# Performance work log

Hardware: AMD Instinct MI355X
Metric: run time of the kernel (lower is better)

## Reference

```python
import jax, jax.numpy as jnp
import numpy as np

BLOCKSIZE = 64  # bitsandbytes default quantization block size

# NF4 codebook (bitsandbytes normal-float 4-bit quantiles)
NF4_CODE = jnp.array([
    -1.0, -0.6961928009986877, -0.5250730514526367, -0.39491748809814453,
    -0.28444138169288635, -0.18477343022823334, -0.09105003625154495, 0.0,
    0.07958029955625534, 0.16093020141124725, 0.24611230194568634,
    0.33791524171829224, 0.44070982933044434, 0.5626170039176941,
    0.7229568362236023, 1.0], dtype=jnp.float32)

IN_FEATURES = 4096
OUT_FEATURES = 16384
TOKENS = 8192  # batch 4 * seq 2048, flattened


def setup_inputs() -> dict:
    key = jax.random.key(0)
    k1, k2, k3, k4 = jax.random.split(key, 4)
    x = jax.random.normal(k1, (TOKENS, IN_FEATURES), dtype=jnp.float32)
    codes = jax.random.randint(k2, (OUT_FEATURES, IN_FEATURES), 0, 16, dtype=jnp.int32)
    n_blocks = OUT_FEATURES * IN_FEATURES // BLOCKSIZE
    absmax = jax.random.uniform(k3, (n_blocks,), dtype=jnp.float32)
    bias = jax.random.normal(k4, (OUT_FEATURES,), dtype=jnp.float32)
    return {"x": x, "codes": codes, "absmax": absmax, "bias": bias}


def _dequant_nf4(codes, absmax):
    # codes: [O, I] int in [0,16); absmax: [O*I/BLOCKSIZE] per-block scale
    O, I = codes.shape
    w = NF4_CODE[codes]                        # [O, I] codebook lookup
    w = w.reshape(-1, BLOCKSIZE) * absmax[:, None]  # block-wise rescale
    return w.reshape(O, I)


def reference(x, codes, absmax, bias):
    w = _dequant_nf4(codes, absmax)            # [O, I]
    return jnp.dot(x, w.T) + bias              # [T, O]
```

## Files before the change

### kernel.cpp

```cpp
#include <hip/hip_runtime.h>
#include <hip/hip_bf16.h>
#include <stdint.h>

#define TOKENS 8192
#define IN_F   4096
#define OUT_F  16384

typedef __bf16 bf16;
typedef __bf16 bf16x8 __attribute__((ext_vector_type(8)));
typedef float  f32x4  __attribute__((ext_vector_type(4)));

__device__ __constant__ float NF4[16] = {
    -1.0f, -0.6961928009986877f, -0.5250730514526367f, -0.39491748809814453f,
    -0.28444138169288635f, -0.18477343022823334f, -0.09105003625154495f, 0.0f,
    0.07958029955625534f, 0.16093020141124725f, 0.24611230194568634f,
    0.33791524171829224f, 0.44070982933044434f, 0.5626170039176941f,
    0.7229568362236023f, 1.0f};

__global__ __launch_bounds__(256) void cvt_kernel(const float* __restrict__ x,
                                                  bf16* __restrict__ xb) {
    size_t base = ((size_t)blockIdx.x * blockDim.x + threadIdx.x) * 8;
    float4 a = *(const float4*)(x + base);
    float4 b = *(const float4*)(x + base + 4);
    bf16x8 w;
    w[0] = (bf16)a.x; w[1] = (bf16)a.y; w[2] = (bf16)a.z; w[3] = (bf16)a.w;
    w[4] = (bf16)b.x; w[5] = (bf16)b.y; w[6] = (bf16)b.z; w[7] = (bf16)b.w;
    *(bf16x8*)(xb + base) = w;
}

__global__ __launch_bounds__(256) void dequant_kernel(const int* __restrict__ codes,
                                                      const float* __restrict__ absmax,
                                                      bf16* __restrict__ W) {
    __shared__ float lut[16];
    if (threadIdx.x < 16) lut[threadIdx.x] = NF4[threadIdx.x];
    __syncthreads();
    size_t base = ((size_t)blockIdx.x * blockDim.x + threadIdx.x) * 8;
    float scale = absmax[base >> 6];
    int4 c0 = *(const int4*)(codes + base);
    int4 c1 = *(const int4*)(codes + base + 4);
    bf16x8 w;
    w[0] = (bf16)(lut[c0.x] * scale);
    w[1] = (bf16)(lut[c0.y] * scale);
    w[2] = (bf16)(lut[c0.z] * scale);
    w[3] = (bf16)(lut[c0.w] * scale);
    w[4] = (bf16)(lut[c1.x] * scale);
    w[5] = (bf16)(lut[c1.y] * scale);
    w[6] = (bf16)(lut[c1.z] * scale);
    w[7] = (bf16)(lut[c1.w] * scale);
    *(bf16x8*)(W + base) = w;
}

typedef const unsigned int __attribute__((address_space(1)))* gas_ptr;
typedef unsigned int __attribute__((address_space(3)))* las_ptr;

__device__ __forceinline__ void async_load16(const void* g, void* l) {
    __builtin_amdgcn_global_load_lds((gas_ptr)(uintptr_t)g, (las_ptr)(uintptr_t)l, 16, 0, 0);
}

#define GBM 256
#define GBN 256
#define GBK 64
#define GNT (IN_F / GBK)

__device__ __forceinline__ void bar_nodrain() {
    __builtin_amdgcn_sched_barrier(0);
    __builtin_amdgcn_s_barrier();
    __builtin_amdgcn_sched_barrier(0);
}

#define CLUSTER(I0, J0)                                                          \
    do {                                                                         \
        __builtin_amdgcn_s_setprio(1);                                           \
        _Pragma("unroll") for (int i_ = 0; i_ < 4; ++i_) {                       \
            _Pragma("unroll") for (int j_ = 0; j_ < 2; ++j_) {                   \
                acc[(I0) + i_][(J0) + j_] = __builtin_amdgcn_mfma_f32_16x16x32_bf16( \
                    a[i_][0], b[(J0) + j_][0], acc[(I0) + i_][(J0) + j_], 0, 0, 0);  \
                acc[(I0) + i_][(J0) + j_] = __builtin_amdgcn_mfma_f32_16x16x32_bf16( \
                    a[i_][1], b[(J0) + j_][1], acc[(I0) + i_][(J0) + j_], 0, 0, 0);  \
            }                                                                    \
        }                                                                        \
        __builtin_amdgcn_s_setprio(0);                                           \
    } while (0)

__global__ __launch_bounds__(512, 2) void gemm256(const bf16* __restrict__ A,
                                                  const bf16* __restrict__ B,
                                                  const float* __restrict__ bias,
                                                  float* __restrict__ C) {
    constexpr int K = IN_F, N = OUT_F;
    extern __shared__ char smem[];

    const int t    = threadIdx.x;
    const int wave = t >> 6, lane = t & 63;
    const int quad = lane >> 4, r16 = lane & 15;
    const int wr = wave >> 2, wc = wave & 3;

    const int g  = blockIdx.x;
    const int s  = (g & 7) * (2048 / 8) + (g >> 3);
    const int by = s >> 6;
    const int bx = s & 63;
    const int m0 = by * GBM;
    const int n0 = bx * GBN;

    const int wl    = wave * 1024 + lane * 16;
    const int fwl   = wl ^ (((wl >> 7) & 7) << 4);
    const int rbase = fwl >> 7;
    const int cbase = (fwl & 127) >> 1;

    const bf16* pA = A + (size_t)(m0 + rbase) * K + cbase;
    const bf16* pB = B + (size_t)(n0 + rbase) * K + cbase;

    char* const sA0 = smem;
    char* const sB0 = smem + 32768;
    char* const sA1 = smem + 65536;
    char* const sB1 = smem + 98304;
    const int wslot = wave * 1024;

#pragma unroll
    for (int h = 0; h < 2; ++h)
#pragma unroll
        for (int i = 0; i < 2; ++i) {
            const size_t go = (size_t)(h * 128 + i * 64) * K;
            const int    lo = h * 16384 + i * 8192 + wslot;
            async_load16(pA + go, sA0 + lo);
            async_load16(pB + go, sB0 + lo);
        }
#pragma unroll
    for (int h = 0; h < 2; ++h)
#pragma unroll
        for (int i = 0; i < 2; ++i) {
            const size_t go = (size_t)(h * 128 + i * 64) * K;
            const int    lo = h * 16384 + i * 8192 + wslot;
            async_load16(pA + GBK + go, sA1 + lo);
            async_load16(pB + GBK + go, sB1 + lo);
        }
    asm volatile("s_waitcnt vmcnt(8)" ::: "memory");
    bar_nodrain();

    const int sw   = (r16 & 7) << 4;
    const int c0   = (quad * 16) ^ sw;
    const int c1   = (64 + quad * 16) ^ sw;
    const int rowA = (wr * 128 + r16) * 128;
    const int rowB = (wc * 64 + r16) * 128;

    f32x4 acc[8][4];
#pragma unroll
    for (int i = 0; i < 8; ++i)
#pragma unroll
        for (int j = 0; j < 4; ++j) acc[i][j] = (f32x4){0.f, 0.f, 0.f, 0.f};

    const bf16* qA = pA + 2 * GBK;
    const bf16* qB = pB + 2 * GBK;

    for (int kt = 0; kt < GNT; ++kt) {
        char* const sA = (kt & 1) ? sA1 : sA0;
        char* const sB = (kt & 1) ? sB1 : sB0;
        const char* rA = sA + rowA;
        const char* rB = sB + rowB;

        bf16x8 a[4][2], b[4][2];
#pragma unroll
        for (int i = 0; i < 4; ++i) {
            a[i][0] = *(const bf16x8*)(rA + i * 2048 + c0);
            a[i][1] = *(const bf16x8*)(rA + i * 2048 + c1);
        }
#pragma unroll
        for (int j = 0; j < 4; ++j) {
            b[j][0] = *(const bf16x8*)(rB + j * 2048 + c0);
            b[j][1] = *(const bf16x8*)(rB + j * 2048 + c1);
        }
        CLUSTER(0, 0);
        CLUSTER(0, 2);
#pragma unroll
        for (int i = 0; i < 4; ++i) {
            a[i][0] = *(const bf16x8*)(rA + (i + 4) * 2048 + c0);
            a[i][1] = *(const bf16x8*)(rA + (i + 4) * 2048 + c1);
        }
        CLUSTER(4, 0);
        bar_nodrain();
        if (kt < GNT - 2) {
#pragma unroll
            for (int h = 0; h < 2; ++h)
#pragma unroll
                for (int i = 0; i < 2; ++i) {
                    const size_t go = (size_t)(h * 128 + i * 64) * K;
                    const int    lo = h * 16384 + i * 8192 + wslot;
                    async_load16(qA + go, sA + lo);
                    async_load16(qB + go, sB + lo);
                }
            qA += GBK; qB += GBK;
        }
        CLUSTER(4, 2);
        if (kt < GNT - 2) {
            asm volatile("s_waitcnt vmcnt(8)" ::: "memory");
            bar_nodrain();
        } else if (kt == GNT - 2) {
            asm volatile("s_waitcnt vmcnt(0)" ::: "memory");
            bar_nodrain();
        }
    }

    float bj[4];
#pragma unroll
    for (int j = 0; j < 4; ++j) bj[j] = bias[n0 + wc * 64 + j * 16 + r16];
#pragma unroll
    for (int i = 0; i < 8; ++i) {
#pragma unroll
        for (int r = 0; r < 4; ++r) {
            const int m = m0 + wr * 128 + i * 16 + quad * 4 + r;
            float* crow = C + (size_t)m * N + n0 + wc * 64 + r16;
#pragma unroll
            for (int j = 0; j < 4; ++j) crow[j * 16] = acc[i][j][r] + bj[j];
        }
    }
}

#define BM 128
#define BN 128
#define BK 32

__global__ __launch_bounds__(256) void gemm_bt(const bf16* __restrict__ A,
                                               const bf16* __restrict__ B,
                                               const float* __restrict__ bias,
                                               float* __restrict__ C) {
    constexpr int M = TOKENS, N = OUT_F, K = IN_F;
    (void)M;
    __shared__ bf16 As[BM * BK];
    __shared__ bf16 Bs[BN * BK];

    const int t = threadIdx.x;
    const int wave = t >> 6, lane = t & 63;
    const int quad = lane >> 4, r16 = lane & 15;
    const int wr = wave >> 1, wc = wave & 1;
    const int m0 = blockIdx.y * BM;
    const int n0 = blockIdx.x * BN;

    f32x4 acc[4][4];
#pragma unroll
    for (int i = 0; i < 4; i++)
#pragma unroll
        for (int j = 0; j < 4; j++) acc[i][j] = (f32x4){0.f, 0.f, 0.f, 0.f};

    const int c0r = t >> 2, c0c = (t & 3) * 8;
    const int c1r = (256 + t) >> 2, c1c = ((256 + t) & 3) * 8;
    bf16* lA0 = As + (size_t)(wave * 64) * 8;
    bf16* lA1 = As + (size_t)(256 + wave * 64) * 8;
    bf16* lB0 = Bs + (size_t)(wave * 64) * 8;
    bf16* lB1 = Bs + (size_t)(256 + wave * 64) * 8;
    const bf16* gA = A + (size_t)m0 * K;
    const bf16* gB = B + (size_t)n0 * K;

    for (int k0 = 0; k0 < K; k0 += BK) {
        async_load16(gA + (size_t)c0r * K + k0 + c0c, lA0);
        async_load16(gA + (size_t)c1r * K + k0 + c1c, lA1);
        async_load16(gB + (size_t)c0r * K + k0 + c0c, lB0);
        async_load16(gB + (size_t)c1r * K + k0 + c1c, lB1);
        __syncthreads();

        bf16x8 af[4], bfr[4];
#pragma unroll
        for (int i = 0; i < 4; i++)
            af[i] = *(const bf16x8*)(As + (wr * 64 + i * 16 + r16) * BK + quad * 8);
#pragma unroll
        for (int j = 0; j < 4; j++)
            bfr[j] = *(const bf16x8*)(Bs + (wc * 64 + j * 16 + r16) * BK + quad * 8);

#pragma unroll
        for (int i = 0; i < 4; i++)
#pragma unroll
            for (int j = 0; j < 4; j++)
                acc[i][j] = __builtin_amdgcn_mfma_f32_16x16x32_bf16(af[i], bfr[j], acc[i][j], 0, 0, 0);
        __syncthreads();
    }

    float bj[4];
#pragma unroll
    for (int j = 0; j < 4; j++) bj[j] = bias[n0 + wc * 64 + j * 16 + r16];
#pragma unroll
    for (int i = 0; i < 4; i++) {
#pragma unroll
        for (int r = 0; r < 4; r++) {
            int m = m0 + wr * 64 + i * 16 + quad * 4 + r;
            float* crow = C + (size_t)m * N + n0 + wc * 64 + r16;
#pragma unroll
            for (int j = 0; j < 4; j++) crow[j * 16] = acc[i][j][r] + bj[j];
        }
    }
}

#define FT 16
__global__ void gemm_fallback(const float* __restrict__ x, const int* __restrict__ codes,
                              const float* __restrict__ absmax, const float* __restrict__ bias,
                              float* __restrict__ C) {
    __shared__ float xs[FT][FT];
    __shared__ float ws_[FT][FT + 1];
    int tx = threadIdx.x, ty = threadIdx.y;
    int n = blockIdx.x * FT + tx;
    int m = blockIdx.y * FT + ty;
    float acc = 0.f;
    for (int k0 = 0; k0 < IN_F; k0 += FT) {
        xs[ty][tx] = x[(size_t)m * IN_F + k0 + tx];
        int o = blockIdx.x * FT + ty;
        size_t widx = (size_t)o * IN_F + k0 + tx;
        ws_[ty][tx] = NF4[codes[widx]] * absmax[widx >> 6];
        __syncthreads();
#pragma unroll
        for (int k = 0; k < FT; k++) acc += xs[ty][k] * ws_[tx][k];
        __syncthreads();
    }
    C[(size_t)m * OUT_F + n] = acc + bias[n];
}

extern "C" void kernel_launch(void* const* d_in, const int* in_sizes, int n_in,
                              void* d_out, int out_size, void* d_ws, size_t ws_size,
                              hipStream_t stream) {
    const float* x      = (const float*)d_in[0];
    const int*   codes  = (const int*)d_in[1];
    const float* absmax = (const float*)d_in[2];
    const float* bias   = (const float*)d_in[3];
    float* out = (float*)d_out;

    const size_t xb_elems = (size_t)TOKENS * IN_F;
    const size_t w_elems  = (size_t)OUT_F * IN_F;
    const size_t need = (xb_elems + w_elems) * sizeof(bf16);

    if (ws_size >= need) {
        bf16* xb = (bf16*)d_ws;
        bf16* W  = xb + xb_elems;
        cvt_kernel<<<(int)(xb_elems / 8 / 256), 256, 0, stream>>>(x, xb);
        dequant_kernel<<<(int)(w_elems / 8 / 256), 256, 0, stream>>>(codes, absmax, W);

        static int smem_ok = -1;
        if (smem_ok < 0) {
            hipError_t e = hipFuncSetAttribute(
                reinterpret_cast<const void*>(gemm256),
                hipFuncAttributeMaxDynamicSharedMemorySize, 131072);
            smem_ok = (e == hipSuccess) ? 1 : 0;
        }
        bool launched = false;
        if (smem_ok) {
            (void)hipGetLastError();
            gemm256<<<dim3(2048), 512, 131072, stream>>>(xb, W, bias, out);
            launched = (hipGetLastError() == hipSuccess);
        }
        if (!launched) {
            gemm_bt<<<dim3(OUT_F / BN, TOKENS / BM), 256, 0, stream>>>(xb, W, bias, out);
        }
    } else {
        gemm_fallback<<<dim3(OUT_F / FT, TOKENS / FT), dim3(FT, FT), 0, stream>>>(
            x, codes, absmax, bias, out);
    }
}
```

Baseline: 1.714 ms.

## Split GEMM k-loop into four barrier-separated phases interleaving LDS reads, async loads, MFMA

```diff
diff --git a/kernel.cpp b/kernel.cpp
--- a/kernel.cpp
+++ b/kernel.cpp
@@ -68,18 +68,25 @@
     __builtin_amdgcn_sched_barrier(0);
 }
 
-#define CLUSTER(I0, J0)                                                          \
-    do {                                                                         \
-        __builtin_amdgcn_s_setprio(1);                                           \
-        _Pragma("unroll") for (int i_ = 0; i_ < 4; ++i_) {                       \
-            _Pragma("unroll") for (int j_ = 0; j_ < 2; ++j_) {                   \
+__device__ __forceinline__ void phase_pre() {
+    __builtin_amdgcn_sched_barrier(0);
+    __builtin_amdgcn_s_barrier();
+    asm volatile("s_waitcnt lgkmcnt(0)" ::: "memory");
+    __builtin_amdgcn_sched_barrier(0);
+}
+
+#define MFMA16(I0, J0)                                                               \
+    do {                                                                             \
+        __builtin_amdgcn_s_setprio(1);                                               \
+        _Pragma("unroll") for (int i_ = 0; i_ < 4; ++i_) {                           \
+            _Pragma("unroll") for (int j_ = 0; j_ < 2; ++j_) {                       \
                 acc[(I0) + i_][(J0) + j_] = __builtin_amdgcn_mfma_f32_16x16x32_bf16( \
                     a[i_][0], b[(J0) + j_][0], acc[(I0) + i_][(J0) + j_], 0, 0, 0);  \
                 acc[(I0) + i_][(J0) + j_] = __builtin_amdgcn_mfma_f32_16x16x32_bf16( \
                     a[i_][1], b[(J0) + j_][1], acc[(I0) + i_][(J0) + j_], 0, 0, 0);  \
-            }                                                                    \
-        }                                                                        \
-        __builtin_amdgcn_s_setprio(0);                                           \
+            }                                                                        \
+        }                                                                            \
+        __builtin_amdgcn_s_setprio(0);                                               \
     } while (0)
 
 __global__ __launch_bounds__(512, 2) void gemm256(const bf16* __restrict__ A,
@@ -151,52 +158,72 @@
     const bf16* qA = pA + 2 * GBK;
     const bf16* qB = pB + 2 * GBK;
 
+#pragma unroll 2
     for (int kt = 0; kt < GNT; ++kt) {
         char* const sA = (kt & 1) ? sA1 : sA0;
         char* const sB = (kt & 1) ? sB1 : sB0;
         const char* rA = sA + rowA;
         const char* rB = sB + rowB;
+        const bool do_stage = (kt < GNT - 2);
 
         bf16x8 a[4][2], b[4][2];
+
 #pragma unroll
         for (int i = 0; i < 4; ++i) {
             a[i][0] = *(const bf16x8*)(rA + i * 2048 + c0);
             a[i][1] = *(const bf16x8*)(rA + i * 2048 + c1);
         }
 #pragma unroll
-        for (int j = 0; j < 4; ++j) {
+        for (int j = 0; j < 2; ++j) {
             b[j][0] = *(const bf16x8*)(rB + j * 2048 + c0);
             b[j][1] = *(const bf16x8*)(rB + j * 2048 + c1);
         }
-        CLUSTER(0, 0);
-        CLUSTER(0, 2);
+        asm volatile("s_waitcnt lgkmcnt(8)" ::: "memory");
+        phase_pre();
+        MFMA16(0, 0);
+        bar_nodrain();
+
+#pragma unroll
+        for (int j = 2; j < 4; ++j) {
+            b[j][0] = *(const bf16x8*)(rB + j * 2048 + c0);
+            b[j][1] = *(const bf16x8*)(rB + j * 2048 + c1);
+        }
+        if (do_stage) {
+            async_load16(qA, sA + wslot);
+            async_load16(qA + (size_t)128 * K, sA + 16384 + wslot);
+        }
+        phase_pre();
+        MFMA16(0, 2);
+        bar_nodrain();
+
 #pragma unroll
         for (int i = 0; i < 4; ++i) {
             a[i][0] = *(const bf16x8*)(rA + (i + 4) * 2048 + c0);
             a[i][1] = *(const bf16x8*)(rA + (i + 4) * 2048 + c1);
         }
-        CLUSTER(4, 0);
+        if (do_stage) {
+            async_load16(qB, sB + wslot);
+            async_load16(qB + (size_t)64 * K, sB + 8192 + wslot);
+            async_load16(qB + (size_t)128 * K, sB + 16384 + wslot);
+            async_load16(qB + (size_t)192 * K, sB + 24576 + wslot);
+        }
+        phase_pre();
+        MFMA16(4, 0);
         bar_nodrain();
-        if (kt < GNT - 2) {
-#pragma unroll
-            for (int h = 0; h < 2; ++h)
-#pragma unroll
-                for (int i = 0; i < 2; ++i) {
-                    const size_t go = (size_t)(h * 128 + i * 64) * K;
-                    const int    lo = h * 16384 + i * 8192 + wslot;
-                    async_load16(qA + go, sA + lo);
-                    async_load16(qB + go, sB + lo);
-                }
+
+        if (do_stage) {
+            async_load16(qA + (size_t)64 * K, sA + 8192 + wslot);
+            async_load16(qA + (size_t)192 * K, sA + 24576 + wslot);
             qA += GBK; qB += GBK;
-        }
-        CLUSTER(4, 2);
-        if (kt < GNT - 2) {
             asm volatile("s_waitcnt vmcnt(8)" ::: "memory");
-            bar_nodrain();
         } else if (kt == GNT - 2) {
             asm volatile("s_waitcnt vmcnt(0)" ::: "memory");
-            bar_nodrain();
-        }
+        }
+        __builtin_amdgcn_sched_barrier(0);
+        __builtin_amdgcn_s_barrier();
+        __builtin_amdgcn_sched_barrier(0);
+        MFMA16(4, 2);
+        bar_nodrain();
     }
 
     float bj[4];
```

New measurement: 1.615 ms. 5.7% less time.
